# Performance work log

Measured on AMD Instinct MI355X. Metric: run time of the kernel, lower is better.

The kernel has to match this reference:

```python
import jax, jax.numpy as jnp
import numpy as np

B, T, E, H, W = 2, 1024, 1024, 8, 31
D = 2 * W + 1  # head dim must equal 2*window_size+1 for the rel-pos broadcast


def _ln(x, w, b):
    mu = jnp.mean(x, axis=-1, keepdims=True)
    var = jnp.mean(jnp.square(x - mu), axis=-1, keepdims=True)
    return (x - mu) * jax.lax.rsqrt(var + 1e-5) * w + b


def setup_inputs() -> dict:
    key = jax.random.key(0)
    k = jax.random.split(key, 8)
    s = 0.02
    return {
        "x": jax.random.normal(k[0], (B, T, E // 2), jnp.float32),
        "ln1_w": jnp.ones(E, jnp.float32), "ln1_b": jnp.zeros(E, jnp.float32),
        "qkv_w": jax.random.normal(k[1], (3 * H * D, E), jnp.float32) * s,
        "qkv_b": jnp.zeros(3 * H * D, jnp.float32),
        "rel_pos": jax.random.normal(k[2], (D, D), jnp.float32) * s,
        "proj_w": jax.random.normal(k[3], (E, H * D), jnp.float32) * s,
        "proj_b": jnp.zeros(E, jnp.float32),
        "ln2_w": jnp.ones(E, jnp.float32), "ln2_b": jnp.zeros(E, jnp.float32),
        "fc_w": jax.random.normal(k[4], (4 * E, E), jnp.float32) * s,
        "fc_b": jnp.zeros(4 * E, jnp.float32),
        "cproj_w": jax.random.normal(k[5], (E, 4 * E), jnp.float32) * s,
        "cproj_b": jnp.zeros(E, jnp.float32),
    }


def reference(x, ln1_w, ln1_b, qkv_w, qkv_b, rel_pos, proj_w, proj_b,
              ln2_w, ln2_b, fc_w, fc_b, cproj_w, cproj_b):
    # --- RotaryEmbedding: angle = x * inv_freq; out = cat(sin, cos) -> [B,T,E]
    dim = 2 * x.shape[-1]
    inv_freq = 1.0 / 10000.0 ** (jnp.arange(0, dim, 2, dtype=jnp.float32) / dim)
    ang = x * inv_freq
    xr = jnp.concatenate([jnp.sin(ang), jnp.cos(ang)], axis=-1)  # [B,T,E]

    # --- custom windowed attention on ln_1(xr)
    h = _ln(xr, ln1_w, ln1_b)
    qkv = h @ qkv_w.T + qkv_b                       # [B,T,3*H*D]
    q, k, v = jnp.split(qkv, 3, axis=-1)

    def heads(t):
        return t.reshape(B, T, H, D).transpose(0, 2, 1, 3)  # [B,H,T,D]

    q, k, v = heads(q), heads(k), heads(v)
    # per-token q-outer-k scores (einsum '...bd,...bv->...bdv'): [B,H,T,D,D]
    scores = jnp.einsum('bhtd,bhtv->bhtdv', q, k)
    # rel-pos bias: Embedding lookup at offsets -W..W (negative indices wrap)
    bias = rel_pos[jnp.arange(-W, W + 1) % D]       # [D, D] == [2W+1, d_model]
    attn = jax.nn.softmax(scores + bias, axis=-2)   # softmax over non-canonical axis
    out = jnp.einsum('bhtdv,bhtv->bhtd', attn, v)   # apply per-token attn matrix to v
    out = out.transpose(0, 2, 1, 3).reshape(B, T, H * D)
    xa = xr + out @ proj_w.T + proj_b               # residual

    # --- MLP
    h2 = _ln(xa, ln2_w, ln2_b)
    m = jax.nn.gelu(h2 @ fc_w.T + fc_b, approximate=False) @ cproj_w.T + cproj_b
    return xa + m
```

## Files before the change

kernel.cpp:

```cpp
#include <hip/hip_runtime.h>
#include <hip/hip_bf16.h>


typedef __bf16 bf16;
typedef bf16 bf16x8 __attribute__((ext_vector_type(8)));
typedef bf16 bf16x4 __attribute__((ext_vector_type(4)));
typedef bf16 bf16x2 __attribute__((ext_vector_type(2)));
typedef float f32x4 __attribute__((ext_vector_type(4)));

__device__ __forceinline__ float rdlane(float x, int l)
{
    return __int_as_float(__builtin_amdgcn_readlane(__float_as_int(x), l));
}

__global__ __launch_bounds__(256) void rotary_ln_kernel(
    const float* __restrict__ x, const float* __restrict__ w,
    const float* __restrict__ b, float* __restrict__ xr, bf16* __restrict__ Y)
{
    const int row = blockIdx.x;
    const int tid = threadIdx.x;
    float2 xv = *(const float2*)(x + (size_t)row * 512 + tid * 2);
    float i0 = exp2f(-(float)(2*tid)     * 0.025952563241307518f);
    float i1 = exp2f(-(float)(2*tid + 1) * 0.025952563241307518f);
    float a0 = xv.x * i0, a1 = xv.y * i1;
    float s0 = sinf(a0), s1 = sinf(a1);
    float c0 = cosf(a0), c1 = cosf(a1);
    *(float2*)(xr + (size_t)row * 1024 + tid*2)       = make_float2(s0, s1);
    *(float2*)(xr + (size_t)row * 1024 + 512 + tid*2) = make_float2(c0, c1);
    float s  = s0 + s1 + c0 + c1;
    float ss = s0*s0 + s1*s1 + c0*c0 + c1*c1;
    #pragma unroll
    for (int off = 32; off > 0; off >>= 1) {
        s  += __shfl_down(s, off);
        ss += __shfl_down(ss, off);
    }
    __shared__ float rs[4], rss[4];
    int wave = tid >> 6, lane = tid & 63;
    if (lane == 0) { rs[wave] = s; rss[wave] = ss; }
    __syncthreads();
    s  = rs[0] + rs[1] + rs[2] + rs[3];
    ss = rss[0] + rss[1] + rss[2] + rss[3];
    float mu   = s * (1.f / 1024.f);
    float var  = ss * (1.f / 1024.f) - mu * mu;
    float rstd = rsqrtf(var + 1e-5f);
    float2 w0 = *(const float2*)(w + tid*2);
    float2 b0 = *(const float2*)(b + tid*2);
    float2 w1 = *(const float2*)(w + 512 + tid*2);
    float2 b1 = *(const float2*)(b + 512 + tid*2);
    bf16x2 y0, y1;
    y0[0] = (bf16)((s0 - mu) * rstd * w0.x + b0.x);
    y0[1] = (bf16)((s1 - mu) * rstd * w0.y + b0.y);
    y1[0] = (bf16)((c0 - mu) * rstd * w1.x + b1.x);
    y1[1] = (bf16)((c1 - mu) * rstd * w1.y + b1.y);
    *(bf16x2*)(Y + (size_t)row * 1024 + tid*2)       = y0;
    *(bf16x2*)(Y + (size_t)row * 1024 + 512 + tid*2) = y1;
}

__device__ __forceinline__ void conv_chunk(
    const float* __restrict__ src, bf16* __restrict__ dst,
    int ci, int N, int K, int Kp)
{
    int kpc = Kp >> 3;
    int r  = ci / kpc;
    int kc = (ci - r * kpc) << 3;
    bf16x8 o;
    if (r < N && kc < K) {
        float4 f0 = *(const float4*)(src + (size_t)r * K + kc);
        float4 f1 = *(const float4*)(src + (size_t)r * K + kc + 4);
        o[0]=(bf16)f0.x; o[1]=(bf16)f0.y; o[2]=(bf16)f0.z; o[3]=(bf16)f0.w;
        o[4]=(bf16)f1.x; o[5]=(bf16)f1.y; o[6]=(bf16)f1.z; o[7]=(bf16)f1.w;
    } else {
        #pragma unroll
        for (int j = 0; j < 8; ++j) o[j] = (bf16)0.f;
    }
    *(bf16x8*)(dst + (size_t)r * Kp + kc) = o;
}

__global__ __launch_bounds__(256) void conv_all_kernel(
    const float* __restrict__ qkv_w, const float* __restrict__ proj_w,
    const float* __restrict__ fc_w,  const float* __restrict__ cproj_w,
    const float* __restrict__ qkv_b,
    bf16* __restrict__ wqkv, bf16* __restrict__ wproj,
    bf16* __restrict__ wfc,  bf16* __restrict__ wcproj,
    float* __restrict__ qkvb_p)
{
    if (blockIdx.x == 5120) {
        for (int i = threadIdx.x; i < 1536; i += 256)
            qkvb_p[i] = (i < 1512) ? qkv_b[i] : 0.f;
        return;
    }
    int idx = blockIdx.x * 256 + threadIdx.x;
    if      (idx < 196608)  conv_chunk(qkv_w,   wqkv,   idx,          1512, 1024, 1024);
    else if (idx < 262144)  conv_chunk(proj_w,  wproj,  idx - 196608, 1024,  504,  512);
    else if (idx < 786432)  conv_chunk(fc_w,    wfc,    idx - 262144, 4096, 1024, 1024);
    else                    conv_chunk(cproj_w, wcproj, idx - 786432, 1024, 4096, 4096);
}

template<int N> __device__ __forceinline__ void vmwait()
{
    if constexpr      (N==0) asm volatile("s_waitcnt vmcnt(0)" ::: "memory");
    else if constexpr (N==2) asm volatile("s_waitcnt vmcnt(2)" ::: "memory");
    else if constexpr (N==3) asm volatile("s_waitcnt vmcnt(3)" ::: "memory");
    else if constexpr (N==4) asm volatile("s_waitcnt vmcnt(4)" ::: "memory");
}
__device__ __forceinline__ void lgkmwait0()
{
    asm volatile("s_waitcnt lgkmcnt(0)" ::: "memory");
}
__device__ __forceinline__ void hw_barrier()
{
    asm volatile("s_barrier" ::: "memory");
}
__device__ __forceinline__ void gload16(const char* src, char* ldsdst)
{
    __builtin_amdgcn_global_load_lds(
        (const __attribute__((address_space(1))) void*)src,
        (__attribute__((address_space(3))) void*)ldsdst, 16, 0, 0);
}
__device__ __forceinline__ float gelu_exact(float v)
{
    return 0.5f * v * (1.f + erff(v * 0.70710678118654752f));
}

template<int EPI>
__global__ __launch_bounds__(512, 4) void gemm11_kernel(
    const bf16* __restrict__ A, const bf16* __restrict__ Wt,
    const float* __restrict__ bias, bf16* __restrict__ Cb,
    int N, int Kp, int ksplit)
{
    __shared__ __align__(16) char lds[3][16384];

    const int tid  = threadIdx.x;
    const int w    = tid >> 6;
    const int lane = tid & 63;
    const int wm   = w >> 2;
    const int wn   = w & 3;
    const int rl   = lane & 15;
    const int slotR = lane >> 4;

    const int gx = gridDim.x, gy = gridDim.y;
    const int nwg = gx * gy * gridDim.z;
    const int chunk = nwg >> 3;
    int id = (blockIdx.z * gy + blockIdx.y) * gx + blockIdx.x;
    int sw = (id & 7) * chunk + (id >> 3);
    const int bx = sw % gx;
    const int t2 = sw / gx;
    const int by = t2 % gy;
    const int bz = t2 / gy;

    const int row0 = by * 128;
    const int col0 = bx * 128;
    const size_t strideBy = (size_t)Kp * 2;
    const size_t kz = (size_t)bz * ksplit * 2;
    const char* Abase = (const char*)A  + (size_t)row0 * strideBy + kz;
    const char* Wbase = (const char*)Wt + (size_t)col0 * strideBy + kz;

    const int r  = tid >> 2;
    const int s  = (tid & 3) ^ ((r >> 1) & 3);
    const size_t srcOff = (size_t)r * strideBy + (size_t)(s << 4);

    f32x4 acc[4][2] = {};

    auto STAGE = [&](int buf, int kt) {
        const char* ab = Abase + (size_t)kt * 64;
        const char* wb = Wbase + (size_t)kt * 64;
        gload16(ab + srcOff, &lds[buf][0]    + tid * 16);
        gload16(wb + srcOff, &lds[buf][8192] + tid * 16);
    };

    const int niter = ksplit >> 5;
    STAGE(0, 0);
    STAGE(1, 1);
    vmwait<2>();
    hw_barrier();

    for (int kt = 0; kt < niter; ++kt) {
        if (kt + 2 < niter) STAGE((kt + 2) % 3, kt + 2);
        const char* base = lds[kt % 3];
        bf16x8 af[4], bfr[2];
        #pragma unroll
        for (int mi = 0; mi < 4; ++mi) {
            int rr = wm * 64 + mi * 16 + rl;
            af[mi] = *(const bf16x8*)
                (base + (rr << 6) + ((slotR ^ ((rr >> 1) & 3)) << 4));
        }
        #pragma unroll
        for (int nj = 0; nj < 2; ++nj) {
            int rr = wn * 32 + nj * 16 + rl;
            bfr[nj] = *(const bf16x8*)
                (base + 8192 + (rr << 6) + ((slotR ^ ((rr >> 1) & 3)) << 4));
        }
        lgkmwait0();
        __builtin_amdgcn_s_setprio(1);
        #pragma unroll
        for (int mi = 0; mi < 4; ++mi)
            #pragma unroll
            for (int nj = 0; nj < 2; ++nj)
                acc[mi][nj] = __builtin_amdgcn_mfma_f32_16x16x32_bf16(
                    af[mi], bfr[nj], acc[mi][nj], 0, 0, 0);
        __builtin_amdgcn_s_setprio(0);

        if (kt + 1 < niter) {
            if (kt + 2 < niter) vmwait<2>();
            else                vmwait<0>();
            hw_barrier();
        }
    }

    const int rq = (lane >> 4) * 4;
    bf16* Cbz = Cb;
    if (EPI == 3) Cbz += (size_t)bz * 2048 * N;
    #pragma unroll
    for (int mi = 0; mi < 4; ++mi) {
        #pragma unroll
        for (int rj = 0; rj < 4; ++rj) {
            int row = row0 + wm * 64 + mi * 16 + rq + rj;
            #pragma unroll
            for (int nj = 0; nj < 2; ++nj) {
                int col = col0 + wn * 32 + nj * 16 + rl;
                float c = acc[mi][nj][rj];
                size_t off = (size_t)row * N + col;
                if (EPI == 1) Cbz[off] = (bf16)gelu_exact(c + bias[col]);
                else          Cbz[off] = (bf16)c;
            }
        }
    }
}

template<int EPI>
__global__ __launch_bounds__(256, 4) void gemm7_kernel(
    const bf16* __restrict__ A, const bf16* __restrict__ Wt,
    const float* __restrict__ bias, bf16* __restrict__ Cb,
    int N, int Kp, int ksplit)
{
    __shared__ __align__(16) char lds[3][12288];

    const int tid  = threadIdx.x;
    const int w    = tid >> 6;
    const int lane = tid & 63;

    const int gx = gridDim.x, gy = gridDim.y;
    const int nwg = gx * gy * gridDim.z;
    const int chunk = nwg >> 3;
    int id = (blockIdx.z * gy + blockIdx.y) * gx + blockIdx.x;
    int sw = (id & 7) * chunk + (id >> 3);
    const int bx = sw % gx;
    const int t2 = sw / gx;
    const int by = t2 % gy;
    const int bz = t2 / gy;

    const int row0 = by * 64;
    const int col0 = bx * 128;
    const int wr = (w >> 1) * 32;
    const int wc = (w & 1) * 64;
    const int rl = lane & 15;
    const int slotR = lane >> 4;

    const size_t strideBy = (size_t)Kp * 2;
    const size_t kz = (size_t)bz * ksplit * 2;
    const char* Abase = (const char*)A  + (size_t)row0 * strideBy + kz;
    const char* Wbase = (const char*)Wt + (size_t)col0 * strideBy + kz;

    const int arow = tid >> 2;
    const size_t srcA0 = (size_t)arow * strideBy
                       + (size_t)(((tid & 3) ^ ((arow >> 1) & 3)) << 4);
    size_t srcB[2];
    #pragma unroll
    for (int i = 0; i < 2; ++i) {
        int o = (i * 256 + tid) * 16;
        int rr = o >> 6;
        int ss = ((o & 63) >> 4) ^ ((rr >> 1) & 3);
        srcB[i] = (size_t)rr * strideBy + (size_t)(ss << 4);
    }

    f32x4 acc[2][4] = {};

    auto STAGE = [&](int buf, int kt) {
        const char* ab = Abase + (size_t)kt * 64;
        const char* wb = Wbase + (size_t)kt * 64;
        gload16(ab + srcA0, &lds[buf][0] + tid * 16);
        #pragma unroll
        for (int i = 0; i < 2; ++i)
            gload16(wb + srcB[i], &lds[buf][4096] + (i * 256 + tid) * 16);
    };

    const int niter = ksplit >> 5;
    STAGE(0, 0);
    STAGE(1, 1);
    vmwait<3>();
    hw_barrier();

    int cur = 0, stg = 2;
    for (int kt = 0; kt < niter; ++kt) {
        if (kt + 2 < niter) STAGE(stg, kt + 2);
        const char* base = lds[cur];
        bf16x8 af[2], bfr[4];
        #pragma unroll
        for (int mi = 0; mi < 2; ++mi) {
            int rr = wr + mi * 16 + rl;
            af[mi] = *(const bf16x8*)
                (base + (rr << 6) + ((slotR ^ ((rr >> 1) & 3)) << 4));
        }
        #pragma unroll
        for (int nj = 0; nj < 4; ++nj) {
            int rr = wc + nj * 16 + rl;
            bfr[nj] = *(const bf16x8*)
                (base + 4096 + (rr << 6) + ((slotR ^ ((rr >> 1) & 3)) << 4));
        }
        __builtin_amdgcn_s_setprio(1);
        #pragma unroll
        for (int mi = 0; mi < 2; ++mi)
            #pragma unroll
            for (int nj = 0; nj < 4; ++nj)
                acc[mi][nj] = __builtin_amdgcn_mfma_f32_16x16x32_bf16(
                    af[mi], bfr[nj], acc[mi][nj], 0, 0, 0);
        __builtin_amdgcn_s_setprio(0);

        if (kt + 1 < niter) {
            lgkmwait0();
            if (kt + 2 < niter) vmwait<3>();
            else                vmwait<0>();
            hw_barrier();
        }
        cur = (cur == 2) ? 0 : cur + 1;
        stg = (stg == 2) ? 0 : stg + 1;
    }

    const int rq = (lane >> 4) * 4;
    bf16* Cbz = Cb;
    if (EPI == 3) Cbz += (size_t)bz * 2048 * N;
    #pragma unroll
    for (int mi = 0; mi < 2; ++mi) {
        #pragma unroll
        for (int rj = 0; rj < 4; ++rj) {
            int row = row0 + wr + mi*16 + rq + rj;
            #pragma unroll
            for (int nj = 0; nj < 4; ++nj) {
                int col = col0 + wc + nj*16 + rl;
                float c = acc[mi][nj][rj];
                size_t off = (size_t)row * N + col;
                if (EPI == 0)      Cbz[off] = (bf16)(c + bias[col]);
                else if (EPI == 1) Cbz[off] = (bf16)gelu_exact(c + bias[col]);
                else               Cbz[off] = (bf16)c;
            }
        }
    }
}

template<int P>
__global__ __launch_bounds__(256) void reduce_kernel(
    const bf16* __restrict__ parts, const float* __restrict__ bias,
    const float* R, float* out)
{
    int row = blockIdx.x;
    int c = threadIdx.x * 4;
    size_t off = (size_t)row * 1024 + c;
    float4 bv = *(const float4*)(bias + c);
    float4 o = *(const float4*)(R + off);
    o.x += bv.x; o.y += bv.y; o.z += bv.z; o.w += bv.w;
    #pragma unroll
    for (int p = 0; p < P; ++p) {
        bf16x4 v = *(const bf16x4*)(parts + (size_t)p * 2048 * 1024 + off);
        o.x += (float)v[0]; o.y += (float)v[1];
        o.z += (float)v[2]; o.w += (float)v[3];
    }
    *(float4*)(out + off) = o;
}

__global__ __launch_bounds__(256) void reduceln_kernel(
    const bf16* __restrict__ parts, const float* __restrict__ bias,
    const float* __restrict__ R, const float* __restrict__ lnw,
    const float* __restrict__ lnb, float* __restrict__ out,
    bf16* __restrict__ Y)
{
    int row = blockIdx.x;
    int c = threadIdx.x * 4;
    size_t off = (size_t)row * 1024 + c;
    float4 bv = *(const float4*)(bias + c);
    float4 o  = *(const float4*)(R + off);
    o.x += bv.x; o.y += bv.y; o.z += bv.z; o.w += bv.w;
    #pragma unroll
    for (int p = 0; p < 2; ++p) {
        bf16x4 v = *(const bf16x4*)(parts + (size_t)p * 2048 * 1024 + off);
        o.x += (float)v[0]; o.y += (float)v[1];
        o.z += (float)v[2]; o.w += (float)v[3];
    }
    *(float4*)(out + off) = o;
    float s  = o.x + o.y + o.z + o.w;
    float ss = o.x*o.x + o.y*o.y + o.z*o.z + o.w*o.w;
    #pragma unroll
    for (int of = 32; of > 0; of >>= 1) {
        s  += __shfl_down(s, of);
        ss += __shfl_down(ss, of);
    }
    __shared__ float rs[4], rss[4];
    int wave = threadIdx.x >> 6, lane = threadIdx.x & 63;
    if (lane == 0) { rs[wave] = s; rss[wave] = ss; }
    __syncthreads();
    s  = rs[0] + rs[1] + rs[2] + rs[3];
    ss = rss[0] + rss[1] + rss[2] + rss[3];
    float mu  = s * (1.f / 1024.f);
    float var = ss * (1.f / 1024.f) - mu * mu;
    float rstd = rsqrtf(var + 1e-5f);
    float4 wv = *(const float4*)(lnw + c);
    float4 lb = *(const float4*)(lnb + c);
    bf16 y[4];
    y[0] = (bf16)((o.x - mu) * rstd * wv.x + lb.x);
    y[1] = (bf16)((o.y - mu) * rstd * wv.y + lb.y);
    y[2] = (bf16)((o.z - mu) * rstd * wv.z + lb.z);
    y[3] = (bf16)((o.w - mu) * rstd * wv.w + lb.w);
    *(uint2*)(Y + (size_t)row * 1024 + c) = *(uint2*)y;
}

__global__ __launch_bounds__(1024) void attn3_kernel(
    const bf16* __restrict__ qkv, const float* __restrict__ rel_pos,
    bf16* __restrict__ outp)
{
    __shared__ float bR[4096];
    __shared__ float bT[4096];
    for (int i = threadIdx.x; i < 4096; i += 1024) {
        int d = i >> 6, v = i & 63;
        float val = (d < 63 && v < 63)
                  ? rel_pos[((d + 32) % 63) * 63 + v] * 1.4426950408889634f
                  : -1e30f;
        bR[(d << 6) + (((v >> 2) ^ (d & 15)) << 2) + (v & 3)] = val;
        bT[(v << 6) + (((d >> 2) ^ (v & 15)) << 2) + (d & 3)] = val;
    }
    __syncthreads();

    const int wave = threadIdx.x >> 6;
    const int lane = threadIdx.x & 63;
    const int tk  = blockIdx.x * 16 + wave;
    const int row = tk >> 3;
    const int h   = tk & 7;
    const bf16* base = qkv + (size_t)row * 1536 + h * 63;
    float q_own = 0.f, k_own = 0.f, v_own = 0.f;
    if (lane < 63) {
        q_own = (float)base[lane] * 1.4426950408889634f;
        k_own = (float)base[504 + lane];
        v_own = (float)base[1008 + lane];
    }

    const float* myT = bT + (lane << 6);
    const int sw = lane & 15;
    float z0 = 0.f, z1 = 0.f, z2 = 0.f, z3 = 0.f;
    #pragma unroll
    for (int g = 0; g < 16; ++g) {
        f32x4 bb = *(const f32x4*)(myT + ((g ^ sw) << 2));
        z0 += __builtin_amdgcn_exp2f(fmaf(rdlane(q_own, 4*g + 0), k_own, bb[0]));
        z1 += __builtin_amdgcn_exp2f(fmaf(rdlane(q_own, 4*g + 1), k_own, bb[1]));
        z2 += __builtin_amdgcn_exp2f(fmaf(rdlane(q_own, 4*g + 2), k_own, bb[2]));
        z3 += __builtin_amdgcn_exp2f(fmaf(rdlane(q_own, 4*g + 3), k_own, bb[3]));
    }
    float Z = (z0 + z1) + (z2 + z3);
    float w_own = (lane < 63) ? v_own / Z : 0.f;

    const float* myR = bR + (lane << 6);
    float a0 = 0.f, a1 = 0.f, a2 = 0.f, a3 = 0.f;
    #pragma unroll
    for (int g = 0; g < 16; ++g) {
        f32x4 bb = *(const f32x4*)(myR + ((g ^ sw) << 2));
        a0 = fmaf(__builtin_amdgcn_exp2f(fmaf(q_own, rdlane(k_own, 4*g + 0), bb[0])),
                  rdlane(w_own, 4*g + 0), a0);
        a1 = fmaf(__builtin_amdgcn_exp2f(fmaf(q_own, rdlane(k_own, 4*g + 1), bb[1])),
                  rdlane(w_own, 4*g + 1), a1);
        a2 = fmaf(__builtin_amdgcn_exp2f(fmaf(q_own, rdlane(k_own, 4*g + 2), bb[2])),
                  rdlane(w_own, 4*g + 2), a2);
        a3 = fmaf(__builtin_amdgcn_exp2f(fmaf(q_own, rdlane(k_own, 4*g + 3), bb[3])),
                  rdlane(w_own, 4*g + 3), a3);
    }
    float acc = (a0 + a1) + (a2 + a3);

    if (lane < 63)
        outp[(size_t)row * 512 + h*63 + lane] = (bf16)acc;
    if (h == 7 && lane == 63) {
        #pragma unroll
        for (int j = 0; j < 8; ++j)
            outp[(size_t)row * 512 + 504 + j] = (bf16)0.f;
    }
}

extern "C" void kernel_launch(void* const* d_in, const int* in_sizes, int n_in,
                              void* d_out, int out_size, void* d_ws, size_t ws_size,
                              hipStream_t stream)
{
    const float* x       = (const float*)d_in[0];
    const float* ln1_w   = (const float*)d_in[1];
    const float* ln1_b   = (const float*)d_in[2];
    const float* qkv_w   = (const float*)d_in[3];
    const float* qkv_b   = (const float*)d_in[4];
    const float* rel_pos = (const float*)d_in[5];
    const float* proj_w  = (const float*)d_in[6];
    const float* proj_b  = (const float*)d_in[7];
    const float* ln2_w   = (const float*)d_in[8];
    const float* ln2_b   = (const float*)d_in[9];
    const float* fc_w    = (const float*)d_in[10];
    const float* fc_b    = (const float*)d_in[11];
    const float* cproj_w = (const float*)d_in[12];
    const float* cproj_b = (const float*)d_in[13];
    float* out = (float*)d_out;

    char* p = (char*)d_ws;
    float* xr      = (float*)p;            p += (size_t)2048*1024*4;
    bf16*  h_bf    = (bf16*)p;             p += (size_t)2048*1024*2;
    bf16*  wqkv    = (bf16*)p;             p += (size_t)1536*1024*2;
    bf16*  wproj   = (bf16*)p;             p += (size_t)1024*512*2;
    bf16*  wfc     = (bf16*)p;             p += (size_t)4096*1024*2;
    bf16*  wcproj  = (bf16*)p;             p += (size_t)1024*4096*2;
    float* qkvb_p  = (float*)p;            p += 8192;
    bf16*  attn_bf = (bf16*)p;             p += (size_t)2048*512*2;
    bf16*  qkvb    = (bf16*)p;
    bf16*  fc_act  = (bf16*)p;
    bf16*  proj_part = qkvb;
    bf16*  cp_part = (bf16*)d_ws;

    conv_all_kernel<<<5121, 256, 0, stream>>>(qkv_w, proj_w, fc_w, cproj_w, qkv_b,
                                              wqkv, wproj, wfc, wcproj, qkvb_p);
    rotary_ln_kernel<<<2048, 256, 0, stream>>>(x, ln1_w, ln1_b, xr, h_bf);
    gemm7_kernel<0><<<dim3(12,32,1), 256, 0, stream>>>(h_bf, wqkv, qkvb_p,
                                                       qkvb, 1536, 1024, 1024);
    attn3_kernel<<<1024, 1024, 0, stream>>>(qkvb, rel_pos, attn_bf);
    gemm7_kernel<3><<<dim3(8,32,2), 256, 0, stream>>>(attn_bf, wproj, nullptr,
                                                      proj_part, 1024, 512, 256);
    reduceln_kernel<<<2048, 256, 0, stream>>>(proj_part, proj_b, xr,
                                              ln2_w, ln2_b, out, h_bf);
    gemm11_kernel<1><<<dim3(32,16,1), 512, 0, stream>>>(h_bf, wfc, fc_b,
                                                        fc_act, 4096, 1024, 1024);
    gemm11_kernel<3><<<dim3(8,16,4), 512, 0, stream>>>(fc_act, wcproj, nullptr,
                                                       cp_part, 1024, 4096, 1024);
    reduce_kernel<4><<<2048, 256, 0, stream>>>(cp_part, cproj_b, out, out);
}
```

Measured before the change: 133.7 us.

## Split-K the MLP GEMMs with double buffering and a separate bias+GELU reduce

The FC GEMM is now split-K by 2 and the cproj GEMM by 8. The GELU epilogue moves into a new reduce kernel that sums the two bf16 partials, adds the bias and applies exact GELU. The GEMM drops from triple to double buffering with __syncthreads and asks for 8 blocks per CU, aiming at more parallelism and occupancy. The cost is much more partial-sum traffic through global memory (bf16 partials), an extra kernel launch, extra bf16 rounding of the partials, and a larger workspace.

```diff
diff --git a/kernel.cpp b/kernel.cpp
--- a/kernel.cpp
+++ b/kernel.cpp
@@ -99,9 +99,7 @@
 template<int N> __device__ __forceinline__ void vmwait()
 {
     if constexpr      (N==0) asm volatile("s_waitcnt vmcnt(0)" ::: "memory");
-    else if constexpr (N==2) asm volatile("s_waitcnt vmcnt(2)" ::: "memory");
     else if constexpr (N==3) asm volatile("s_waitcnt vmcnt(3)" ::: "memory");
-    else if constexpr (N==4) asm volatile("s_waitcnt vmcnt(4)" ::: "memory");
 }
 __device__ __forceinline__ void lgkmwait0()
 {
@@ -123,12 +121,11 @@
 }
 
 template<int EPI>
-__global__ __launch_bounds__(512, 4) void gemm11_kernel(
+__global__ __launch_bounds__(512, 8) void gemm11b_kernel(
     const bf16* __restrict__ A, const bf16* __restrict__ Wt,
-    const float* __restrict__ bias, bf16* __restrict__ Cb,
-    int N, int Kp, int ksplit)
-{
-    __shared__ __align__(16) char lds[3][16384];
+    bf16* __restrict__ Cb, int N, int Kp, int ksplit)
+{
+    __shared__ __align__(16) char lds[2][16384];
 
     const int tid  = threadIdx.x;
     const int w    = tid >> 6;
@@ -170,13 +167,11 @@
 
     const int niter = ksplit >> 5;
     STAGE(0, 0);
-    STAGE(1, 1);
-    vmwait<2>();
-    hw_barrier();
-
+    __syncthreads();
     for (int kt = 0; kt < niter; ++kt) {
-        if (kt + 2 < niter) STAGE((kt + 2) % 3, kt + 2);
-        const char* base = lds[kt % 3];
+        if (kt + 1 < niter)
+            STAGE((kt + 1) & 1, kt + 1);
+        const char* base = lds[kt & 1];
         bf16x8 af[4], bfr[2];
         #pragma unroll
         for (int mi = 0; mi < 4; ++mi) {
@@ -190,7 +185,6 @@
             bfr[nj] = *(const bf16x8*)
                 (base + 8192 + (rr << 6) + ((slotR ^ ((rr >> 1) & 3)) << 4));
         }
-        lgkmwait0();
         __builtin_amdgcn_s_setprio(1);
         #pragma unroll
         for (int mi = 0; mi < 4; ++mi)
@@ -199,17 +193,11 @@
                 acc[mi][nj] = __builtin_amdgcn_mfma_f32_16x16x32_bf16(
                     af[mi], bfr[nj], acc[mi][nj], 0, 0, 0);
         __builtin_amdgcn_s_setprio(0);
-
-        if (kt + 1 < niter) {
-            if (kt + 2 < niter) vmwait<2>();
-            else                vmwait<0>();
-            hw_barrier();
-        }
+        __syncthreads();
     }
 
     const int rq = (lane >> 4) * 4;
-    bf16* Cbz = Cb;
-    if (EPI == 3) Cbz += (size_t)bz * 2048 * N;
+    bf16* Cbz = Cb + (size_t)bz * 2048 * N;
     #pragma unroll
     for (int mi = 0; mi < 4; ++mi) {
         #pragma unroll
@@ -218,10 +206,8 @@
             #pragma unroll
             for (int nj = 0; nj < 2; ++nj) {
                 int col = col0 + wn * 32 + nj * 16 + rl;
-                float c = acc[mi][nj][rj];
                 size_t off = (size_t)row * N + col;
-                if (EPI == 1) Cbz[off] = (bf16)gelu_exact(c + bias[col]);
-                else          Cbz[off] = (bf16)c;
+                Cbz[off] = (bf16)acc[mi][nj][rj];
             }
         }
     }
@@ -365,6 +351,28 @@
         o.z += (float)v[2]; o.w += (float)v[3];
     }
     *(float4*)(out + off) = o;
+}
+
+__global__ __launch_bounds__(256) void reduce_gelu_kernel(
+    const bf16* __restrict__ parts, const float* __restrict__ bias,
+    bf16* __restrict__ out)
+{
+    size_t base = ((size_t)blockIdx.x * 256 + threadIdx.x) * 8;
+    int col = (int)(base & 4095);
+    bf16x8 p0 = *(const bf16x8*)(parts + base);
+    bf16x8 p1 = *(const bf16x8*)(parts + (size_t)2048 * 4096 + base);
+    float4 b0 = *(const float4*)(bias + col);
+    float4 b1 = *(const float4*)(bias + col + 4);
+    bf16x8 o;
+    o[0] = (bf16)gelu_exact((float)p0[0] + (float)p1[0] + b0.x);
+    o[1] = (bf16)gelu_exact((float)p0[1] + (float)p1[1] + b0.y);
+    o[2] = (bf16)gelu_exact((float)p0[2] + (float)p1[2] + b0.z);
+    o[3] = (bf16)gelu_exact((float)p0[3] + (float)p1[3] + b0.w);
+    o[4] = (bf16)gelu_exact((float)p0[4] + (float)p1[4] + b1.x);
+    o[5] = (bf16)gelu_exact((float)p0[5] + (float)p1[5] + b1.y);
+    o[6] = (bf16)gelu_exact((float)p0[6] + (float)p1[6] + b1.z);
+    o[7] = (bf16)gelu_exact((float)p0[7] + (float)p1[7] + b1.w);
+    *(bf16x8*)(out + base) = o;
 }
 
 __global__ __launch_bounds__(256) void reduceln_kernel(
@@ -509,10 +517,11 @@
     bf16*  wcproj  = (bf16*)p;             p += (size_t)1024*4096*2;
     float* qkvb_p  = (float*)p;            p += 8192;
     bf16*  attn_bf = (bf16*)p;             p += (size_t)2048*512*2;
-    bf16*  qkvb    = (bf16*)p;
-    bf16*  fc_act  = (bf16*)p;
+    bf16*  qkvb    = (bf16*)p;             p += (size_t)2048*1536*2;
+    bf16*  fc_act  = (bf16*)p;             p += (size_t)2048*4096*2;
     bf16*  proj_part = qkvb;
-    bf16*  cp_part = (bf16*)d_ws;
+    bf16*  fc_part = (bf16*)p;             p += (size_t)2*2048*4096*2;
+    bf16*  cp_part = (bf16*)p;             p += (size_t)8*2048*1024*2;
 
     conv_all_kernel<<<5121, 256, 0, stream>>>(qkv_w, proj_w, fc_w, cproj_w, qkv_b,
                                               wqkv, wproj, wfc, wcproj, qkvb_p);
@@ -524,9 +533,10 @@
                                                       proj_part, 1024, 512, 256);
     reduceln_kernel<<<2048, 256, 0, stream>>>(proj_part, proj_b, xr,
                                               ln2_w, ln2_b, out, h_bf);
-    gemm11_kernel<1><<<dim3(32,16,1), 512, 0, stream>>>(h_bf, wfc, fc_b,
-                                                        fc_act, 4096, 1024, 1024);
-    gemm11_kernel<3><<<dim3(8,16,4), 512, 0, stream>>>(fc_act, wcproj, nullptr,
-                                                       cp_part, 1024, 4096, 1024);
-    reduce_kernel<4><<<2048, 256, 0, stream>>>(cp_part, cproj_b, out, out);
-}
+    gemm11b_kernel<3><<<dim3(32,16,2), 512, 0, stream>>>(h_bf, wfc,
+                                                         fc_part, 4096, 1024, 512);
+    reduce_gelu_kernel<<<4096, 256, 0, stream>>>(fc_part, fc_b, fc_act);
+    gemm11b_kernel<3><<<dim3(8,16,8), 512, 0, stream>>>(fc_act, wcproj,
+                                                        cp_part, 1024, 4096, 512);
+    reduce_kernel<8><<<2048, 256, 0, stream>>>(cp_part, cproj_b, out, out);
+}
```

New measurement: 148.5 us. 1.11x slower.
